# Kernel tuning notes

Hardware: AMD Instinct MI355X
Metric: run time of the kernel (lower is better)

## Reference

```python
import jax, jax.numpy as jnp
import numpy as np

N = 4_000_000
POINT_DIM = 2
FEAT_OUT = 64
NUM_SEGMENTS = 4096


def setup_inputs() -> dict:
    key = jax.random.key(0)
    k1, k2, k3, k4 = jax.random.split(key, 4)
    x = jax.random.normal(k1, (N, POINT_DIM), dtype=jnp.float32)
    segment_ids = jnp.sort(jax.random.randint(k2, (N,), 0, NUM_SEGMENTS, dtype=jnp.int64 if jax.config.jax_enable_x64 else jnp.int32))
    W = jax.random.normal(k3, (POINT_DIM, FEAT_OUT), dtype=jnp.float32) / np.sqrt(POINT_DIM)
    b = jax.random.normal(k4, (FEAT_OUT,), dtype=jnp.float32)
    return {"x": x, "segment_ids": segment_ids, "W": W, "b": b, "num_segments": NUM_SEGMENTS}


def reference(x, segment_ids, W, b, num_segments):
    # phi: per-point linear projection, [N, point_dim] -> [N, feat_out]
    h = x @ W + b
    # 'add' aggregation over each set == segment sum (ids are sorted per-set)
    out = jax.ops.segment_sum(h, segment_ids, num_segments=num_segments,
                              indices_are_sorted=True)
    return out  # [num_segments, feat_out]
```

## Files before the change

### kernel.cpp

```cpp
#include <hip/hip_runtime.h>
#include <stdint.h>

#define NSEG 4096


__global__ __launch_bounds__(256) void seg_reduce(
    const float4* __restrict__ x4,
    const int4*   __restrict__ ids4,
    float* __restrict__ acc,
    int nchunk, int nchunk_w)
{
    const int lane = threadIdx.x & 63;
    const int stride = gridDim.x * blockDim.x;

    for (int chunk = blockIdx.x * blockDim.x + threadIdx.x; chunk < nchunk_w; chunk += stride) {
        const bool valid = chunk < nchunk;

        int4 idA, idB;
        float4 xA, xB, xC, xD;
        if (valid) {
            idA = ids4[2 * chunk];
            idB = ids4[2 * chunk + 1];
            xA = x4[4 * chunk + 0];
            xB = x4[4 * chunk + 1];
            xC = x4[4 * chunk + 2];
            xD = x4[4 * chunk + 3];
        } else {
            idA = make_int4(-1, -1, -1, -1);
            idB = idA;
            xA = make_float4(0.f, 0.f, 0.f, 0.f);
            xB = xC = xD = xA;
        }

        int   cur = idA.x;
        float s0 = xA.x, s1 = xA.y, cnt = valid ? 1.f : 0.f;

        #define PROC(SEG, X0, X1)                                          \
            if ((SEG) != cur) {                                            \
                if (cur >= 0) {                                            \
                    atomicAdd(&acc[4 * cur + 0], s0);                      \
                    atomicAdd(&acc[4 * cur + 1], s1);                      \
                    atomicAdd(&acc[4 * cur + 2], cnt);                     \
                }                                                          \
                cur = (SEG); s0 = (X0); s1 = (X1); cnt = 1.f;              \
            } else {                                                       \
                s0 += (X0); s1 += (X1); cnt += valid ? 1.f : 0.f;          \
            }

        PROC(idA.y, xA.z, xA.w)
        PROC(idA.z, xB.x, xB.y)
        PROC(idA.w, xB.z, xB.w)
        PROC(idB.x, xC.x, xC.y)
        PROC(idB.y, xC.z, xC.w)
        PROC(idB.z, xD.x, xD.y)
        PROC(idB.w, xD.z, xD.w)
        #undef PROC

        int prev = __shfl_up(cur, 1);
        bool head = (lane == 0) || (prev != cur);
        uint64_t heads = __ballot(head);
        uint64_t below = heads & (~0ull >> (63 - lane));
        int run_start = 63 - __builtin_clzll(below);

        #pragma unroll
        for (int d = 1; d < 64; d <<= 1) {
            float t0 = __shfl_up(s0, d);
            float t1 = __shfl_up(s1, d);
            float tc = __shfl_up(cnt, d);
            if (lane - d >= run_start) { s0 += t0; s1 += t1; cnt += tc; }
        }

        bool tail = (lane == 63) || ((heads >> (lane + 1)) & 1ull);
        if (tail && cur >= 0) {
            atomicAdd(&acc[4 * cur + 0], s0);
            atomicAdd(&acc[4 * cur + 1], s1);
            atomicAdd(&acc[4 * cur + 2], cnt);
        }
    }
}

__global__ __launch_bounds__(256) void epilogue(
    const float* __restrict__ acc,
    const float* __restrict__ W,
    const float* __restrict__ b,
    float* __restrict__ out)
{
    int idx = blockIdx.x * blockDim.x + threadIdx.x;
    int s = idx >> 6;
    int f = idx & 63;
    out[idx] = acc[4 * s] * W[f] + acc[4 * s + 1] * W[64 + f] + acc[4 * s + 2] * b[f];
}

extern "C" void kernel_launch(void* const* d_in, const int* in_sizes, int n_in,
                              void* d_out, int out_size, void* d_ws, size_t ws_size,
                              hipStream_t stream) {
    const float4* x4   = (const float4*)d_in[0];
    const int4*   ids4 = (const int4*)d_in[1];
    const float*  W    = (const float*)d_in[2];
    const float*  b    = (const float*)d_in[3];
    float* out = (float*)d_out;

    const int n = in_sizes[1];
    const int nchunk = n / 8;
    const int nchunk_w = (nchunk + 63) & ~63;

    float* acc = (float*)d_ws;

    hipMemsetAsync(d_ws, 0, 4 * NSEG * sizeof(float), stream);

    seg_reduce<<<2048, 256, 0, stream>>>(x4, ids4, acc, nchunk, nchunk_w);
    epilogue<<<(NSEG * 64) / 256, 256, 0, stream>>>(acc, W, b, out);
}
```

Baseline: 91.42 us.

## Process 16 points per thread with one-pass grid and uniform-segment fast path

Each thread now handles 16 points instead of 8, and the grid-stride loop is replaced by a single pass over a grid sized to the data. A fast path skips the per-element segment comparison when all 16 ids in a thread's chunk are equal. The epilogue is vectorized to float4 writes. The bigger per-thread load uses more registers, and the fast path adds a branch that can diverge within a wave.

```diff
diff --git a/kernel.cpp b/kernel.cpp
--- a/kernel.cpp
+++ b/kernel.cpp
@@ -8,87 +8,106 @@
     const float4* __restrict__ x4,
     const int4*   __restrict__ ids4,
     float* __restrict__ acc,
-    int nchunk, int nchunk_w)
+    int nchunk)
 {
     const int lane = threadIdx.x & 63;
-    const int stride = gridDim.x * blockDim.x;
+    const int idx = blockIdx.x * blockDim.x + threadIdx.x;
+    const bool valid = idx < nchunk;
 
-    for (int chunk = blockIdx.x * blockDim.x + threadIdx.x; chunk < nchunk_w; chunk += stride) {
-        const bool valid = chunk < nchunk;
+    int4 id0, id1, id2, id3;
+    float4 xv[8];
+    if (valid) {
+        id0 = ids4[4 * idx + 0];
+        id1 = ids4[4 * idx + 1];
+        id2 = ids4[4 * idx + 2];
+        id3 = ids4[4 * idx + 3];
+        #pragma unroll
+        for (int i = 0; i < 8; ++i) xv[i] = x4[8 * idx + i];
+    } else {
+        id0 = make_int4(-1, -1, -1, -1);
+        id1 = id0; id2 = id0; id3 = id0;
+        #pragma unroll
+        for (int i = 0; i < 8; ++i) xv[i] = make_float4(0.f, 0.f, 0.f, 0.f);
+    }
 
-        int4 idA, idB;
-        float4 xA, xB, xC, xD;
-        if (valid) {
-            idA = ids4[2 * chunk];
-            idB = ids4[2 * chunk + 1];
-            xA = x4[4 * chunk + 0];
-            xB = x4[4 * chunk + 1];
-            xC = x4[4 * chunk + 2];
-            xD = x4[4 * chunk + 3];
-        } else {
-            idA = make_int4(-1, -1, -1, -1);
-            idB = idA;
-            xA = make_float4(0.f, 0.f, 0.f, 0.f);
-            xB = xC = xD = xA;
+    int cur;
+    float s0, s1, cnt;
+
+    if (id0.x == id3.w) {
+        cur = id0.x;
+        float a0 = 0.f, a1 = 0.f;
+        #pragma unroll
+        for (int i = 0; i < 8; ++i) {
+            a0 += xv[i].x + xv[i].z;
+            a1 += xv[i].y + xv[i].w;
         }
+        s0 = a0; s1 = a1;
+        cnt = valid ? 16.f : 0.f;
+    } else {
+        int segs[16];
+        segs[0] = id0.x;  segs[1] = id0.y;  segs[2] = id0.z;  segs[3] = id0.w;
+        segs[4] = id1.x;  segs[5] = id1.y;  segs[6] = id1.z;  segs[7] = id1.w;
+        segs[8] = id2.x;  segs[9] = id2.y;  segs[10] = id2.z; segs[11] = id2.w;
+        segs[12] = id3.x; segs[13] = id3.y; segs[14] = id3.z; segs[15] = id3.w;
+        float p0[16], p1[16];
+        #pragma unroll
+        for (int i = 0; i < 8; ++i) {
+            p0[2 * i]     = xv[i].x;  p1[2 * i]     = xv[i].y;
+            p0[2 * i + 1] = xv[i].z;  p1[2 * i + 1] = xv[i].w;
+        }
+        cur = segs[0]; s0 = p0[0]; s1 = p1[0]; cnt = 1.f;
+        #pragma unroll
+        for (int i = 1; i < 16; ++i) {
+            if (segs[i] != cur) {
+                atomicAdd(&acc[4 * cur + 0], s0);
+                atomicAdd(&acc[4 * cur + 1], s1);
+                atomicAdd(&acc[4 * cur + 2], cnt);
+                cur = segs[i]; s0 = p0[i]; s1 = p1[i]; cnt = 1.f;
+            } else {
+                s0 += p0[i]; s1 += p1[i]; cnt += 1.f;
+            }
+        }
+    }
 
-        int   cur = idA.x;
-        float s0 = xA.x, s1 = xA.y, cnt = valid ? 1.f : 0.f;
+    int prev = __shfl_up(cur, 1);
+    bool head = (lane == 0) || (prev != cur);
+    uint64_t heads = __ballot(head);
+    uint64_t below = heads & (~0ull >> (63 - lane));
+    int run_start = 63 - __builtin_clzll(below);
 
-        #define PROC(SEG, X0, X1)                                          \
-            if ((SEG) != cur) {                                            \
-                if (cur >= 0) {                                            \
-                    atomicAdd(&acc[4 * cur + 0], s0);                      \
-                    atomicAdd(&acc[4 * cur + 1], s1);                      \
-                    atomicAdd(&acc[4 * cur + 2], cnt);                     \
-                }                                                          \
-                cur = (SEG); s0 = (X0); s1 = (X1); cnt = 1.f;              \
-            } else {                                                       \
-                s0 += (X0); s1 += (X1); cnt += valid ? 1.f : 0.f;          \
-            }
+    #pragma unroll
+    for (int d = 1; d < 64; d <<= 1) {
+        float t0 = __shfl_up(s0, d);
+        float t1 = __shfl_up(s1, d);
+        float tc = __shfl_up(cnt, d);
+        if (lane - d >= run_start) { s0 += t0; s1 += t1; cnt += tc; }
+    }
 
-        PROC(idA.y, xA.z, xA.w)
-        PROC(idA.z, xB.x, xB.y)
-        PROC(idA.w, xB.z, xB.w)
-        PROC(idB.x, xC.x, xC.y)
-        PROC(idB.y, xC.z, xC.w)
-        PROC(idB.z, xD.x, xD.y)
-        PROC(idB.w, xD.z, xD.w)
-        #undef PROC
-
-        int prev = __shfl_up(cur, 1);
-        bool head = (lane == 0) || (prev != cur);
-        uint64_t heads = __ballot(head);
-        uint64_t below = heads & (~0ull >> (63 - lane));
-        int run_start = 63 - __builtin_clzll(below);
-
-        #pragma unroll
-        for (int d = 1; d < 64; d <<= 1) {
-            float t0 = __shfl_up(s0, d);
-            float t1 = __shfl_up(s1, d);
-            float tc = __shfl_up(cnt, d);
-            if (lane - d >= run_start) { s0 += t0; s1 += t1; cnt += tc; }
-        }
-
-        bool tail = (lane == 63) || ((heads >> (lane + 1)) & 1ull);
-        if (tail && cur >= 0) {
-            atomicAdd(&acc[4 * cur + 0], s0);
-            atomicAdd(&acc[4 * cur + 1], s1);
-            atomicAdd(&acc[4 * cur + 2], cnt);
-        }
+    bool tail = (lane == 63) || ((heads >> (lane + 1)) & 1ull);
+    if (tail && cur >= 0) {
+        atomicAdd(&acc[4 * cur + 0], s0);
+        atomicAdd(&acc[4 * cur + 1], s1);
+        atomicAdd(&acc[4 * cur + 2], cnt);
     }
 }
 
 __global__ __launch_bounds__(256) void epilogue(
-    const float* __restrict__ acc,
-    const float* __restrict__ W,
-    const float* __restrict__ b,
-    float* __restrict__ out)
+    const float*  __restrict__ acc,
+    const float4* __restrict__ W4,
+    const float4* __restrict__ b4,
+    float4* __restrict__ out4)
 {
     int idx = blockIdx.x * blockDim.x + threadIdx.x;
-    int s = idx >> 6;
-    int f = idx & 63;
-    out[idx] = acc[4 * s] * W[f] + acc[4 * s + 1] * W[64 + f] + acc[4 * s + 2] * b[f];
+    int s = idx >> 4;
+    int f = idx & 15;
+    float a0 = acc[4 * s], a1 = acc[4 * s + 1], c = acc[4 * s + 2];
+    float4 w0 = W4[f], w1 = W4[16 + f], bb = b4[f];
+    float4 o;
+    o.x = a0 * w0.x + a1 * w1.x + c * bb.x;
+    o.y = a0 * w0.y + a1 * w1.y + c * bb.y;
+    o.z = a0 * w0.z + a1 * w1.z + c * bb.z;
+    o.w = a0 * w0.w + a1 * w1.w + c * bb.w;
+    out4[idx] = o;
 }
 
 extern "C" void kernel_launch(void* const* d_in, const int* in_sizes, int n_in,
@@ -96,18 +115,17 @@
                               hipStream_t stream) {
     const float4* x4   = (const float4*)d_in[0];
     const int4*   ids4 = (const int4*)d_in[1];
-    const float*  W    = (const float*)d_in[2];
-    const float*  b    = (const float*)d_in[3];
-    float* out = (float*)d_out;
+    const float4* W4   = (const float4*)d_in[2];
+    const float4* b4   = (const float4*)d_in[3];
+    float4* out4 = (float4*)d_out;
 
     const int n = in_sizes[1];
-    const int nchunk = n / 8;
-    const int nchunk_w = (nchunk + 63) & ~63;
+    const int nchunk = n / 16;
+    const int nblocks = (nchunk + 255) / 256;
 
     float* acc = (float*)d_ws;
 
     hipMemsetAsync(d_ws, 0, 4 * NSEG * sizeof(float), stream);
-
-    seg_reduce<<<2048, 256, 0, stream>>>(x4, ids4, acc, nchunk, nchunk_w);
-    epilogue<<<(NSEG * 64) / 256, 256, 0, stream>>>(acc, W, b, out);
+    seg_reduce<<<nblocks, 256, 0, stream>>>(x4, ids4, acc, nchunk);
+    epilogue<<<(NSEG * 64 / 4) / 256, 256, 0, stream>>>(acc, W4, b4, out4);
 }
```

Result: no change. 92.34 us (+1.0%).
